# Optimization experiments

Measured on AMD Instinct MI355X. Metric: run time of the kernel, lower is better.

Reference implementation:

```python
import jax, jax.numpy as jnp
import numpy as np

EMBED_DIM = 256
EPS = 1e-5  # torch F.instance_norm default eps


def setup_inputs() -> dict:
    key = jax.random.key(0)
    ks = jax.random.split(key, 11)
    B, Nq, Nm, C = 4, 4096, 4096, EMBED_DIM
    s = 1.0 / np.sqrt(C)
    return {
        "query": jax.random.normal(ks[0], (B, Nq, C), jnp.float32),
        "key": jax.random.normal(ks[1], (B, Nm, C), jnp.float32),
        "value": jax.random.normal(ks[2], (B, Nm, C), jnp.float32),
        "Wq": jax.random.normal(ks[3], (C, C), jnp.float32) * s,
        "bq": jnp.zeros((C,), jnp.float32),
        "Wk": jax.random.normal(ks[4], (C, C), jnp.float32) * s,
        "bk": jnp.zeros((C,), jnp.float32),
        "Wv": jax.random.normal(ks[5], (C, C), jnp.float32) * s,
        "bv": jnp.zeros((C,), jnp.float32),
        "Wm": jax.random.normal(ks[6], (C, C), jnp.float32) * s,
        "bm": jnp.zeros((C,), jnp.float32),
    }


def reference(query, key, value, Wq, bq, Wk, bk, Wv, bv, Wm, bm):
    # Linear projections (torch nn.Linear: x @ W.T + b)
    q = query @ Wq.T + bq   # [B, Nq, C]
    k = key @ Wk.T + bk     # [B, Nm, C]
    v = value @ Wv.T + bv   # [B, Nm, C]

    attn = jnp.einsum('bnc,bmc->bnm', q, k)  # [B, Nq, Nm]

    # F.instance_norm on [B, Nq, Nm]: N=B, C=Nq, spatial=Nm -> normalize each
    # row over the last dim with biased variance, eps=1e-5, no affine.
    mu = jnp.mean(attn, axis=-1, keepdims=True)
    var = jnp.mean(jnp.square(attn - mu), axis=-1, keepdims=True)
    attn = (attn - mu) * jax.lax.rsqrt(var + EPS)

    # use_softmax=True branch
    attn = attn * (EMBED_DIM ** -0.5)
    attn = jax.nn.softmax(attn, axis=-1)

    out = jnp.einsum('bnm,bmc->bnc', attn, v)  # [B, Nq, C]

    # add_residual=True branch
    return (query + out) @ Wm.T + bm
```

## Files before the change

### kernel.cpp

```cpp
#include <hip/hip_runtime.h>
#include <hip/hip_bf16.h>
#include <cmath>

#define CD 256
#define NQ 4096
#define NM 4096
#define NB 4
#define NTOT (NB*NQ)

typedef __bf16 bf16;
typedef __attribute__((ext_vector_type(8))) __bf16 bf16x8;
typedef __attribute__((ext_vector_type(4))) __bf16 bf16x4;
typedef __attribute__((ext_vector_type(4))) float f32x4;

#define MFMA(a,b,c) __builtin_amdgcn_mfma_f32_16x16x32_bf16(a,b,c,0,0,0)

__global__ __launch_bounds__(256) void cvt_w_kernel(
    const float* __restrict__ wq, const float* __restrict__ wk,
    const float* __restrict__ wv, const float* __restrict__ wm,
    bf16* __restrict__ out)
{
    int i = (blockIdx.x*256 + threadIdx.x)*4;
    const float* srcs[4] = {wq, wk, wv, wm};
    #pragma unroll
    for (int m=0;m<4;++m){
        f32x4 v = *(const f32x4*)(srcs[m]+i);
        bf16x4 o;
        #pragma unroll
        for (int e=0;e<4;++e) o[e] = (bf16)v[e];
        *(bf16x4*)(out + m*65536 + i) = o;
    }
}

template<int MODE>
__global__ __launch_bounds__(256) void proj_kernel(
    const float* __restrict__ X, const bf16* __restrict__ W,
    const float* __restrict__ bias, bf16* __restrict__ out, bf16* __restrict__ out2)
{
    const int wave = threadIdx.x>>6, lane = threadIdx.x&63;
    const int lr = lane&15, lg = lane>>4;
    const int n0 = (blockIdx.x>>2)*64 + wave*16;
    const int co0 = (blockIdx.x&3)*64;

    bf16x8 xf[8];
    {
        const float* xr = X + (size_t)(n0+lr)*CD + lg*8;
        #pragma unroll
        for (int ch=0; ch<8; ++ch){
            f32x4 a = *(const f32x4*)(xr + ch*32);
            f32x4 b = *(const f32x4*)(xr + ch*32 + 4);
            bf16x8 t;
            #pragma unroll
            for (int e=0;e<4;++e){ t[e]=(bf16)a[e]; t[4+e]=(bf16)b[e]; }
            xf[ch]=t;
        }
    }
    f32x4 acc[4], acc2[4];
    #pragma unroll
    for (int t=0;t<4;++t){ acc[t]=(f32x4){0,0,0,0}; acc2[t]=(f32x4){0,0,0,0}; }

    #pragma unroll
    for (int t=0;t<4;++t){
        const bf16* wr = W + (size_t)(co0+t*16+lr)*CD + lg*8;
        #pragma unroll
        for (int ch=0; ch<8; ++ch){
            bf16x8 wf = *(const bf16x8*)(wr + ch*32);
            if (MODE==0)      acc[t]  = MFMA(wf, xf[ch], acc[t]);
            else if (MODE==1) acc2[t] = MFMA(xf[ch], wf, acc2[t]);
            else {            acc[t]  = MFMA(wf, xf[ch], acc[t]);
                              acc2[t] = MFMA(xf[ch], wf, acc2[t]); }
        }
    }

    if (MODE==0 || MODE==2){
        const int n = n0 + lr;
        #pragma unroll
        for (int t=0;t<4;++t){
            int co = co0 + t*16 + 4*lg;
            bf16x4 o;
            #pragma unroll
            for (int r=0;r<4;++r) o[r] = (bf16)(acc[t][r] + bias[co+r]);
            *(bf16x4*)(out + (size_t)n*CD + co) = o;
        }
    }
    if (MODE==1 || MODE==2){
        const int b = n0 / NM;
        const int m0 = (n0 % NM) + 4*lg;
        #pragma unroll
        for (int t=0;t<4;++t){
            int co = co0 + t*16 + lr;
            float bb = bias[co];
            bf16x4 o;
            #pragma unroll
            for (int r=0;r<4;++r) o[r] = (bf16)(acc2[t][r] + bb);
            *(bf16x4*)(out2 + (size_t)b*CD*NM + (size_t)co*NM + m0) = o;
        }
    }
}

__global__ __launch_bounds__(256) void ksum_kernel(
    const bf16* __restrict__ kt, float* __restrict__ ksum)
{
    const int wave = threadIdx.x>>6, lane = threadIdx.x&63;
    const int b = blockIdx.x>>6, c = (blockIdx.x&63)*4 + wave;
    const bf16* row = kt + (size_t)b*CD*NM + (size_t)c*NM;
    float s = 0.0f;
    #pragma unroll
    for (int i=0;i<8;++i){
        bf16x8 v = *(const bf16x8*)(row + (i*64+lane)*8);
        #pragma unroll
        for (int e=0;e<8;++e) s += (float)v[e];
    }
    #pragma unroll
    for (int off=1; off<64; off<<=1) s += __shfl_xor(s, off);
    if (lane==0) ksum[b*256 + c] = s;
}

__global__ __launch_bounds__(256) void gram_kernel(
    const bf16* __restrict__ kt, float* __restrict__ gpart)
{
    const int wave = threadIdx.x>>6, lane = threadIdx.x&63;
    const int lr = lane&15, lg = lane>>4;
    const int b = blockIdx.x>>5, ct = (blockIdx.x>>3)&3, jc = blockIdx.x&7;
    const bf16* ktb = kt + (size_t)b*CD*NM;
    const int c0 = ct*64 + wave*16;

    f32x4 acc[16];
    #pragma unroll
    for (int t=0;t<16;++t) acc[t]=(f32x4){0,0,0,0};

    for (int it=0; it<16; ++it){
        const int j0 = jc*512 + it*32;
        bf16x8 af = *(const bf16x8*)(ktb + (size_t)(c0+lr)*NM + j0 + lg*8);
        #pragma unroll
        for (int t=0;t<16;++t){
            bf16x8 bfr = *(const bf16x8*)(ktb + (size_t)(t*16+lr)*NM + j0 + lg*8);
            acc[t] = MFMA(af, bfr, acc[t]);
        }
    }
    #pragma unroll
    for (int t=0;t<16;++t){
        #pragma unroll
        for (int r=0;r<4;++r){
            int c  = c0 + 4*lg + r;
            int cp = t*16 + lr;
            gpart[(((size_t)jc*4 + b)*256 + c)*256 + cp] = acc[t][r];
        }
    }
}

__global__ __launch_bounds__(256) void gfin_kernel(
    const float* __restrict__ gpart, bf16* __restrict__ gbf)
{
    int gid = blockIdx.x*256 + threadIdx.x;
    int b = gid>>16, idx = gid&65535;
    float s = 0.0f;
    #pragma unroll
    for (int jc=0;jc<8;++jc) s += gpart[((size_t)jc*4 + b)*65536 + idx];
    gbf[(size_t)b*65536 + idx] = (bf16)s;
}

__global__ __launch_bounds__(256) void rowstats_kernel(
    const bf16* __restrict__ q, const bf16* __restrict__ gbf,
    const float* __restrict__ ksumg, float* __restrict__ stats)
{
    __shared__ float ksum[256];
    const int wave = threadIdx.x>>6, lane = threadIdx.x&63;
    const int lr = lane&15, lg = lane>>4;
    const int n0 = blockIdx.x*64;
    const int b = n0 / NQ;
    const int row16 = n0 + wave*16;
    ksum[threadIdx.x] = ksumg[b*256 + threadIdx.x];
    __syncthreads();

    bf16x8 qf[8];
    const bf16* qr = q + (size_t)(row16+lr)*CD + lg*8;
    #pragma unroll
    for (int ch=0; ch<8; ++ch) qf[ch] = *(const bf16x8*)(qr + ch*32);

    const bf16* gb = gbf + (size_t)b*65536;
    f32x4 acc[16];
    #pragma unroll
    for (int t=0;t<16;++t) acc[t]=(f32x4){0,0,0,0};
    #pragma unroll
    for (int t=0;t<16;++t){
        #pragma unroll
        for (int ch=0; ch<8; ++ch){
            bf16x8 bf = *(const bf16x8*)&gb[(size_t)(t*16+lr)*256 + ch*32 + lg*8];
            acc[t] = MFMA(qf[ch], bf, acc[t]);
        }
    }
    float msq[4]={0,0,0,0}, mean[4]={0,0,0,0};
    #pragma unroll
    for (int t=0;t<16;++t){
        float ks = ksum[t*16+lr];
        #pragma unroll
        for (int r=0;r<4;++r){
            float qv = (float)q[(size_t)(row16+4*lg+r)*CD + t*16+lr];
            msq[r]  = fmaf(acc[t][r], qv, msq[r]);
            mean[r] = fmaf(qv, ks, mean[r]);
        }
    }
    #pragma unroll
    for (int off=1; off<16; off<<=1){
        #pragma unroll
        for (int r=0;r<4;++r){
            msq[r]  += __shfl_xor(msq[r], off);
            mean[r] += __shfl_xor(mean[r], off);
        }
    }
    if (lr==0){
        #pragma unroll
        for (int r=0;r<4;++r){
            int row = row16 + 4*lg + r;
            float mu = mean[r]*(1.0f/NM);
            float ms = msq[r]*(1.0f/NM);
            float var = ms - mu*mu;
            float rstd = rsqrtf(fmaxf(var,0.0f) + 1e-5f);
            float a2 = rstd * (1.0f/16.0f) * 1.4426950408889634f;
            stats[row*2+0] = mu*a2;
            stats[row*2+1] = a2;
        }
    }
}

__global__ __launch_bounds__(512) void flash_kernel(
    const bf16* __restrict__ q, const bf16* __restrict__ k,
    const bf16* __restrict__ vt, const float* __restrict__ stats,
    bf16* __restrict__ opart, float* __restrict__ dpart)
{
    __shared__ __align__(16) bf16 K_lds[64][264];
    __shared__ __align__(16) bf16 P_lds[128][72];
    const int wave = threadIdx.x>>6, lane = threadIdx.x&63;
    const int lr = lane&15, lg = lane>>4;
    const int qt = blockIdx.x>>2, slice = blockIdx.x&3;
    const int n0 = qt*128;
    const int b = n0 / NQ;
    const bf16* kb = k  + (size_t)b*NM*CD;
    const bf16* vb = vt + (size_t)b*CD*NM + (size_t)(wave*32)*NM;
    const int row16 = n0 + wave*16;

    bf16x8 qf[8];
    const bf16* qr = q + (size_t)(row16+lr)*CD + lg*8;
    #pragma unroll
    for (int ch=0; ch<8; ++ch) qf[ch] = *(const bf16x8*)(qr + ch*32);

    float c2r[4], a2r[4];
    #pragma unroll
    for (int r=0;r<4;++r){
        int row = row16 + 4*lg + r;
        c2r[r] = stats[row*2+0];
        a2r[r] = stats[row*2+1];
    }

    f32x4 oacc[8][2];
    #pragma unroll
    for (int rt=0;rt<8;++rt){ oacc[rt][0]=(f32x4){0,0,0,0}; oacc[rt][1]=(f32x4){0,0,0,0}; }
    float denom[4]={0,0,0,0};

    const int jbeg = slice*(NM/4);
    bf16x8 kreg[4];
    #pragma unroll
    for (int p=0;p<4;++p){
        int f = threadIdx.x + p*512;
        kreg[p] = *(const bf16x8*)(kb + (size_t)(jbeg + (f>>5))*CD + (f&31)*8);
    }
    for (int it=0; it<16; ++it){
        const int j0 = jbeg + it*64;
        #pragma unroll
        for (int p=0;p<4;++p){
            int f = threadIdx.x + p*512;
            *(bf16x8*)&K_lds[f>>5][(f&31)*8] = kreg[p];
        }
        __syncthreads();
        if (it < 15){
            #pragma unroll
            for (int p=0;p<4;++p){
                int f = threadIdx.x + p*512;
                kreg[p] = *(const bf16x8*)(kb + (size_t)(j0+64 + (f>>5))*CD + (f&31)*8);
            }
        }
        f32x4 s0=(f32x4){0,0,0,0}, s1=(f32x4){0,0,0,0};
        f32x4 s2=(f32x4){0,0,0,0}, s3=(f32x4){0,0,0,0};
        #pragma unroll
        for (int ch=0; ch<8; ++ch){
            s0 = MFMA(qf[ch], *(const bf16x8*)&K_lds[     lr][lg*8+ch*32], s0);
            s1 = MFMA(qf[ch], *(const bf16x8*)&K_lds[16+lr][lg*8+ch*32], s1);
            s2 = MFMA(qf[ch], *(const bf16x8*)&K_lds[32+lr][lg*8+ch*32], s2);
            s3 = MFMA(qf[ch], *(const bf16x8*)&K_lds[48+lr][lg*8+ch*32], s3);
        }
        #pragma unroll
        for (int r=0;r<4;++r){
            float p0 = exp2f(s0[r]*a2r[r] - c2r[r]);
            float p1 = exp2f(s1[r]*a2r[r] - c2r[r]);
            float p2 = exp2f(s2[r]*a2r[r] - c2r[r]);
            float p3 = exp2f(s3[r]*a2r[r] - c2r[r]);
            denom[r] += (p0 + p1) + (p2 + p3);
            int prow = wave*16 + 4*lg + r;
            P_lds[prow][lr]    = (bf16)p0;
            P_lds[prow][16+lr] = (bf16)p1;
            P_lds[prow][32+lr] = (bf16)p2;
            P_lds[prow][48+lr] = (bf16)p3;
        }
        __syncthreads();
        #pragma unroll
        for (int w=0; w<2; ++w){
            bf16x8 vf0 = *(const bf16x8*)(vb + (size_t)lr*NM      + j0 + w*32 + lg*8);
            bf16x8 vf1 = *(const bf16x8*)(vb + (size_t)(16+lr)*NM + j0 + w*32 + lg*8);
            #pragma unroll
            for (int rt=0;rt<8;++rt){
                bf16x8 pf = *(const bf16x8*)&P_lds[rt*16+lr][w*32+lg*8];
                oacc[rt][0] = MFMA(pf, vf0, oacc[rt][0]);
                oacc[rt][1] = MFMA(pf, vf1, oacc[rt][1]);
            }
        }
    }

    #pragma unroll
    for (int off=1; off<16; off<<=1){
        #pragma unroll
        for (int r=0;r<4;++r) denom[r] += __shfl_xor(denom[r], off);
    }
    if (lr==0){
        #pragma unroll
        for (int r=0;r<4;++r)
            dpart[(size_t)slice*NTOT + row16 + 4*lg + r] = denom[r];
    }
    #pragma unroll
    for (int rt=0;rt<8;++rt){
        #pragma unroll
        for (int ct=0;ct<2;++ct){
            #pragma unroll
            for (int r=0;r<4;++r){
                int row = n0 + rt*16 + 4*lg + r;
                int co  = wave*32 + ct*16 + lr;
                opart[((size_t)slice*NTOT + row)*CD + co] = (bf16)oacc[rt][ct][r];
            }
        }
    }
}

__global__ __launch_bounds__(256) void dinv_kernel(
    const float* __restrict__ dpart, float* __restrict__ dinv)
{
    int row = blockIdx.x*256 + threadIdx.x;
    dinv[row] = 1.0f / (dpart[row] + dpart[NTOT+row]
                      + dpart[2*(size_t)NTOT+row] + dpart[3*(size_t)NTOT+row]);
}

__global__ __launch_bounds__(256) void final_kernel(
    const bf16* __restrict__ opart, const float* __restrict__ dinv,
    const float* __restrict__ query, const bf16* __restrict__ W,
    const float* __restrict__ bias, float* __restrict__ out)
{
    const int wave = threadIdx.x>>6, lane = threadIdx.x&63;
    const int lr = lane&15, lg = lane>>4;
    const int n0 = (blockIdx.x>>2)*64 + wave*16;
    const int co0 = (blockIdx.x&3)*64;
    const int n = n0 + lr;
    const float di = dinv[n];

    bf16x8 uf[8];
    #pragma unroll
    for (int ch=0; ch<8; ++ch){
        const int c = lg*8 + ch*32;
        float a[8];
        f32x4 qa = *(const f32x4*)(query + (size_t)n*CD + c);
        f32x4 qb = *(const f32x4*)(query + (size_t)n*CD + c + 4);
        #pragma unroll
        for (int e=0;e<4;++e){ a[e]=qa[e]; a[4+e]=qb[e]; }
        #pragma unroll
        for (int s=0;s<4;++s){
            bf16x8 o = *(const bf16x8*)&opart[((size_t)s*NTOT + n)*CD + c];
            #pragma unroll
            for (int e=0;e<8;++e) a[e] = fmaf((float)o[e], di, a[e]);
        }
        bf16x8 t;
        #pragma unroll
        for (int e=0;e<8;++e) t[e] = (bf16)a[e];
        uf[ch] = t;
    }

    f32x4 acc[4];
    #pragma unroll
    for (int t=0;t<4;++t) acc[t]=(f32x4){0,0,0,0};
    #pragma unroll
    for (int t=0;t<4;++t){
        const bf16* wr = W + (size_t)(co0+t*16+lr)*CD + lg*8;
        #pragma unroll
        for (int ch=0; ch<8; ++ch)
            acc[t] = MFMA(*(const bf16x8*)(wr+ch*32), uf[ch], acc[t]);
    }
    #pragma unroll
    for (int t=0;t<4;++t){
        int co = co0 + t*16 + 4*lg;
        f32x4 o;
        #pragma unroll
        for (int r=0;r<4;++r) o[r] = acc[t][r] + bias[co+r];
        *(f32x4*)(out + (size_t)n*CD + co) = o;
    }
}

extern "C" void kernel_launch(void* const* d_in, const int* in_sizes, int n_in,
                              void* d_out, int out_size, void* d_ws, size_t ws_size,
                              hipStream_t stream)
{
    const float* query = (const float*)d_in[0];
    const float* key_  = (const float*)d_in[1];
    const float* value = (const float*)d_in[2];
    const float* Wq = (const float*)d_in[3];
    const float* bq = (const float*)d_in[4];
    const float* Wk = (const float*)d_in[5];
    const float* bk = (const float*)d_in[6];
    const float* Wv = (const float*)d_in[7];
    const float* bv = (const float*)d_in[8];
    const float* Wm = (const float*)d_in[9];
    const float* bm = (const float*)d_in[10];
    float* out = (float*)d_out;

    bf16* wsb = (bf16*)d_ws;
    bf16* wqb = wsb;
    bf16* wkb = wqb + 65536;
    bf16* wvb = wkb + 65536;
    bf16* wmb = wvb + 65536;
    bf16* qbuf  = wsb + 4*65536;
    bf16* kbuf  = qbuf  + (size_t)NTOT*CD;
    bf16* vtbuf = kbuf  + (size_t)NTOT*CD;
    float* statsbuf = (float*)(vtbuf + (size_t)NTOT*CD);
    float* ksumbuf  = statsbuf + (size_t)NTOT*2;
    float* dinvbuf  = ksumbuf + 1024;
    bf16*  gbf      = (bf16*)(dinvbuf + NTOT);
    float* dpart    = (float*)(gbf + (size_t)4*65536);
    bf16*  opart    = (bf16*)(dpart + (size_t)NTOT*4);
    bf16*  ktbuf    = opart;
    float* gpart    = (float*)(opart + (size_t)4*NTOT*CD);

    cvt_w_kernel<<<64,256,0,stream>>>(Wq, Wk, Wv, Wm, wsb);
    proj_kernel<0><<<1024,256,0,stream>>>(query, wqb, bq, qbuf,  nullptr);
    proj_kernel<2><<<1024,256,0,stream>>>(key_,  wkb, bk, kbuf,  ktbuf);
    proj_kernel<1><<<1024,256,0,stream>>>(value, wvb, bv, nullptr, vtbuf);
    ksum_kernel<<<256,256,0,stream>>>(ktbuf, ksumbuf);
    gram_kernel<<<128,256,0,stream>>>(ktbuf, gpart);
    gfin_kernel<<<1024,256,0,stream>>>(gpart, gbf);
    rowstats_kernel<<<256,256,0,stream>>>(qbuf, gbf, ksumbuf, statsbuf);
    flash_kernel<<<512,512,0,stream>>>(qbuf, kbuf, vtbuf, statsbuf, opart, dpart);
    dinv_kernel<<<64,256,0,stream>>>(dpart, dinvbuf);
    final_kernel<<<1024,256,0,stream>>>(opart, dinvbuf, query, wmb, bm, out);
}
```

Baseline: 407.1 us.

## Double-buffer K and P tiles in flash kernel, remap projection block order

Measured after the change: 398.2 us. 2.2% less time.

```diff
diff --git a/kernel.cpp b/kernel.cpp
--- a/kernel.cpp
+++ b/kernel.cpp
@@ -39,8 +39,8 @@
 {
     const int wave = threadIdx.x>>6, lane = threadIdx.x&63;
     const int lr = lane&15, lg = lane>>4;
-    const int n0 = (blockIdx.x>>2)*64 + wave*16;
-    const int co0 = (blockIdx.x&3)*64;
+    const int n0 = (blockIdx.x & 255)*64 + wave*16;
+    const int co0 = (blockIdx.x >> 8)*64;
 
     bf16x8 xf[8];
     {
@@ -229,8 +229,8 @@
     const bf16* __restrict__ vt, const float* __restrict__ stats,
     bf16* __restrict__ opart, float* __restrict__ dpart)
 {
-    __shared__ __align__(16) bf16 K_lds[64][264];
-    __shared__ __align__(16) bf16 P_lds[128][72];
+    __shared__ __align__(16) bf16 K_lds[2][64][264];
+    __shared__ __align__(16) bf16 P_lds[2][128][72];
     const int wave = threadIdx.x>>6, lane = threadIdx.x&63;
     const int lr = lane&15, lg = lane>>4;
     const int qt = blockIdx.x>>2, slice = blockIdx.x&3;
@@ -260,61 +260,67 @@
 
     const int jbeg = slice*(NM/4);
     bf16x8 kreg[4];
-    #pragma unroll
-    for (int p=0;p<4;++p){
-        int f = threadIdx.x + p*512;
-        kreg[p] = *(const bf16x8*)(kb + (size_t)(jbeg + (f>>5))*CD + (f&31)*8);
-    }
-    for (int it=0; it<16; ++it){
-        const int j0 = jbeg + it*64;
-        #pragma unroll
-        for (int p=0;p<4;++p){
-            int f = threadIdx.x + p*512;
-            *(bf16x8*)&K_lds[f>>5][(f&31)*8] = kreg[p];
-        }
+
+#define LOADK(JJ) { _Pragma("unroll") \
+    for (int p=0;p<4;++p){ int f = threadIdx.x + p*512; \
+        kreg[p] = *(const bf16x8*)(kb + (size_t)((JJ) + (f>>5))*CD + (f&31)*8); } }
+#define WRITEK(BB) { _Pragma("unroll") \
+    for (int p=0;p<4;++p){ int f = threadIdx.x + p*512; \
+        *(bf16x8*)&K_lds[BB][f>>5][(f&31)*8] = kreg[p]; } }
+#define QK(BB) { \
+    f32x4 s0=(f32x4){0,0,0,0}, s1=(f32x4){0,0,0,0}; \
+    f32x4 s2=(f32x4){0,0,0,0}, s3=(f32x4){0,0,0,0}; \
+    _Pragma("unroll") \
+    for (int ch=0; ch<8; ++ch){ \
+        s0 = MFMA(qf[ch], *(const bf16x8*)&K_lds[BB][     lr][lg*8+ch*32], s0); \
+        s1 = MFMA(qf[ch], *(const bf16x8*)&K_lds[BB][16+lr][lg*8+ch*32], s1); \
+        s2 = MFMA(qf[ch], *(const bf16x8*)&K_lds[BB][32+lr][lg*8+ch*32], s2); \
+        s3 = MFMA(qf[ch], *(const bf16x8*)&K_lds[BB][48+lr][lg*8+ch*32], s3); \
+    } \
+    _Pragma("unroll") \
+    for (int r=0;r<4;++r){ \
+        float p0 = exp2f(s0[r]*a2r[r] - c2r[r]); \
+        float p1 = exp2f(s1[r]*a2r[r] - c2r[r]); \
+        float p2 = exp2f(s2[r]*a2r[r] - c2r[r]); \
+        float p3 = exp2f(s3[r]*a2r[r] - c2r[r]); \
+        denom[r] += (p0 + p1) + (p2 + p3); \
+        int prow = wave*16 + 4*lg + r; \
+        P_lds[BB][prow][lr]    = (bf16)p0; \
+        P_lds[BB][prow][16+lr] = (bf16)p1; \
+        P_lds[BB][prow][32+lr] = (bf16)p2; \
+        P_lds[BB][prow][48+lr] = (bf16)p3; \
+    } }
+#define PV(BB, J0) { _Pragma("unroll") \
+    for (int w=0; w<2; ++w){ \
+        bf16x8 vf0 = *(const bf16x8*)(vb + (size_t)lr*NM      + (J0) + w*32 + lg*8); \
+        bf16x8 vf1 = *(const bf16x8*)(vb + (size_t)(16+lr)*NM + (J0) + w*32 + lg*8); \
+        _Pragma("unroll") \
+        for (int rt=0;rt<8;++rt){ \
+            bf16x8 pf = *(const bf16x8*)&P_lds[BB][rt*16+lr][w*32+lg*8]; \
+            oacc[rt][0] = MFMA(pf, vf0, oacc[rt][0]); \
+            oacc[rt][1] = MFMA(pf, vf1, oacc[rt][1]); \
+        } } }
+
+    LOADK(jbeg);
+    WRITEK(0);
+    __syncthreads();
+    QK(0);
+    LOADK(jbeg + 64);
+
+    for (int t=0; t<16; ++t){
+        const int j0 = jbeg + t*64;
+        if (t < 15) WRITEK((t+1)&1);
         __syncthreads();
-        if (it < 15){
-            #pragma unroll
-            for (int p=0;p<4;++p){
-                int f = threadIdx.x + p*512;
-                kreg[p] = *(const bf16x8*)(kb + (size_t)(j0+64 + (f>>5))*CD + (f&31)*8);
-            }
-        }
-        f32x4 s0=(f32x4){0,0,0,0}, s1=(f32x4){0,0,0,0};
-        f32x4 s2=(f32x4){0,0,0,0}, s3=(f32x4){0,0,0,0};
-        #pragma unroll
-        for (int ch=0; ch<8; ++ch){
-            s0 = MFMA(qf[ch], *(const bf16x8*)&K_lds[     lr][lg*8+ch*32], s0);
-            s1 = MFMA(qf[ch], *(const bf16x8*)&K_lds[16+lr][lg*8+ch*32], s1);
-            s2 = MFMA(qf[ch], *(const bf16x8*)&K_lds[32+lr][lg*8+ch*32], s2);
-            s3 = MFMA(qf[ch], *(const bf16x8*)&K_lds[48+lr][lg*8+ch*32], s3);
-        }
-        #pragma unroll
-        for (int r=0;r<4;++r){
-            float p0 = exp2f(s0[r]*a2r[r] - c2r[r]);
-            float p1 = exp2f(s1[r]*a2r[r] - c2r[r]);
-            float p2 = exp2f(s2[r]*a2r[r] - c2r[r]);
-            float p3 = exp2f(s3[r]*a2r[r] - c2r[r]);
-            denom[r] += (p0 + p1) + (p2 + p3);
-            int prow = wave*16 + 4*lg + r;
-            P_lds[prow][lr]    = (bf16)p0;
-            P_lds[prow][16+lr] = (bf16)p1;
-            P_lds[prow][32+lr] = (bf16)p2;
-            P_lds[prow][48+lr] = (bf16)p3;
-        }
-        __syncthreads();
-        #pragma unroll
-        for (int w=0; w<2; ++w){
-            bf16x8 vf0 = *(const bf16x8*)(vb + (size_t)lr*NM      + j0 + w*32 + lg*8);
-            bf16x8 vf1 = *(const bf16x8*)(vb + (size_t)(16+lr)*NM + j0 + w*32 + lg*8);
-            #pragma unroll
-            for (int rt=0;rt<8;++rt){
-                bf16x8 pf = *(const bf16x8*)&P_lds[rt*16+lr][w*32+lg*8];
-                oacc[rt][0] = MFMA(pf, vf0, oacc[rt][0]);
-                oacc[rt][1] = MFMA(pf, vf1, oacc[rt][1]);
-            }
-        }
-    }
+        PV(t&1, j0);
+        if (t < 15){
+            if (t < 14) LOADK(jbeg + (t+2)*64);
+            QK((t+1)&1);
+        }
+    }
+#undef LOADK
+#undef WRITEK
+#undef QK
+#undef PV
 
     #pragma unroll
     for (int off=1; off<16; off<<=1){
@@ -355,8 +361,8 @@
 {
     const int wave = threadIdx.x>>6, lane = threadIdx.x&63;
     const int lr = lane&15, lg = lane>>4;
-    const int n0 = (blockIdx.x>>2)*64 + wave*16;
-    const int co0 = (blockIdx.x&3)*64;
+    const int n0 = (blockIdx.x & 255)*64 + wave*16;
+    const int co0 = (blockIdx.x >> 8)*64;
     const int n = n0 + lr;
     const float di = dinv[n];
 
```
